# Performance work log

Hardware: AMD Instinct MI355X
Metric: run time of the kernel (lower is better)

## Reference

```python
import jax, jax.numpy as jnp
import numpy as np

B, S, D, H = 2, 2048, 1024, 4
DK = D // H


def setup_inputs() -> dict:
    key = jax.random.key(0)
    ks = jax.random.split(key, 12)
    inp = {
        "Q_input": jax.random.normal(ks[0], (B, S, D), jnp.float32),
        "K": jax.random.normal(ks[1], (B, S, D), jnp.float32),
        "V": jax.random.normal(ks[2], (B, S, D), jnp.float32),
        "T_field": jax.random.normal(ks[3], (32, 32, 16, 16), jnp.float32),
        "Wq_w": jax.random.normal(ks[4], (D, D), jnp.float32) * 0.02,
        "Wq_b": jnp.zeros((D,), jnp.float32),
        "Wo_w": jax.random.normal(ks[5], (D, D), jnp.float32) * 0.02,
        "Wo_b": jnp.zeros((D,), jnp.float32),
        "proj_w": jax.random.normal(ks[6], (24, DK), jnp.float32) * 0.02,
        "proj_b": jnp.zeros((24,), jnp.float32),
        "geo_w": jnp.ones((4,), jnp.float32),
        "temperature": jnp.asarray(1.0, jnp.float32),
    }
    return inp


def _psi(x, proj_w, proj_b):
    # x: (B,H,S,DK) -> 16D real biquaternion via (A,B,Theta) -> A*exp(Th)+B*exp(i*Th)
    gen = x @ proj_w.T + proj_b                      # (B,H,S,24)
    A, Bg = gen[..., 0:8], gen[..., 8:16]
    Th = jnp.clip(gen[..., 16:24], -8.0, 8.0)
    psi_real = A * jnp.exp(Th) + Bg * jnp.cos(Th)
    psi_imag = Bg * jnp.sin(Th)
    return jnp.concatenate([psi_real, psi_imag], axis=-1)  # (B,H,S,16)


def reference(Q_input, K, V, T_field, Wq_w, Wq_b, Wo_w, Wo_b, proj_w, proj_b, geo_w, temperature):
    b, sq, d = Q_input.shape
    sk = K.shape[1]
    dk = d // H
    Q = (Q_input @ Wq_w.T + Wq_b).reshape(b, sq, H, dk).transpose(0, 2, 1, 3)
    Kh = K.reshape(b, sk, H, dk).transpose(0, 2, 1, 3)
    Vh = V.reshape(b, sk, H, dk).transpose(0, 2, 1, 3)
    pq = _psi(Q, proj_w, proj_b)   # (b,H,sq,16)
    pk = _psi(Kh, proj_w, proj_b)  # (b,H,sk,16)
    qr, qi = pq[..., :8], pq[..., 8:]
    kr, ki = pk[..., :8], pk[..., 8:]
    # tensor: real part of complex inner product; spinor: imaginary (rotational) part
    tensor = jnp.einsum('bhqd,bhkd->bhqk', qr, kr) + jnp.einsum('bhqd,bhkd->bhqk', qi, ki)
    spinor = jnp.einsum('bhqd,bhkd->bhqk', qr, ki) - jnp.einsum('bhqd,bhkd->bhqk', qi, kr)
    qn2 = jnp.sum(pq * pq, -1)  # (b,H,sq)
    kn2 = jnp.sum(pk * pk, -1)  # (b,H,sk)
    gram = qn2[..., :, None] * kn2[..., None, :]
    # wedge: antisymmetric span magnitude (Gram residual)
    wedge = jnp.sqrt(jnp.maximum(gram - tensor**2 - spinor**2, 0.0) + 1e-6)
    # hodge: amplitude contraction (rank-2 -> rank-1 conservation)
    hodge = jnp.sqrt(qn2 + 1e-6)[..., :, None] * jnp.sqrt(kn2 + 1e-6)[..., None, :]
    scores = (geo_w[0] * wedge + geo_w[1] * tensor + geo_w[2] * spinor + geo_w[3] * hodge) / 4.0
    scores = scores / temperature
    w = jax.nn.softmax(scores, axis=-1)              # dropout disabled (eval)
    out = jnp.einsum('bhqk,bhkd->bhqd', w, Vh)
    out = out.transpose(0, 2, 1, 3).reshape(b, sq, d)
    return out @ Wo_w.T + Wo_b
```

## Files before the change

### kernel.cpp

```cpp
#include <hip/hip_runtime.h>
#include <hip/hip_bf16.h>
#include <math.h>

#define B_ 2
#define S_ 2048
#define D_ 1024
#define H_ 4
#define DK_ 256
#define NJ 24
#define NG 96
#define KTA 128
#define NT2 (S_ / KTA)
#define NTL (NT2 / 2)

typedef _Float16 f16;
typedef _Float16 f16x2 __attribute__((ext_vector_type(2)));
typedef _Float16 f16x4 __attribute__((ext_vector_type(4)));
typedef _Float16 f16x8 __attribute__((ext_vector_type(8)));
typedef float f32x16 __attribute__((ext_vector_type(16)));
typedef float v2f __attribute__((ext_vector_type(2)));

__global__ __launch_bounds__(256) void k_prep(
    const float* __restrict__ Wq_w, const float* __restrict__ proj_w,
    const float* __restrict__ Wq_b, const float* __restrict__ proj_b,
    const float* __restrict__ Wo_w, const float* __restrict__ V,
    f16* __restrict__ Mf, f16* __restrict__ Mkf,
    float* __restrict__ cbias, float* __restrict__ pbias,
    f16* __restrict__ Wf, f16* __restrict__ Vt2) {
  __shared__ f16 tile[64][72];
  const int bid = blockIdx.x;
  const int t = threadIdx.x;
  if (bid < 384) {
    int tid = bid * 256 + t;
    int hj = tid >> 10, d = tid & 1023;
    int h = hj / NJ, j = hj - h * NJ;
    const float* wq = Wq_w + (size_t)(h * DK_) * D_ + d;
    const float* pw = proj_w + j * DK_;
    float acc = 0.f;
#pragma unroll 8
    for (int k = 0; k < DK_; ++k) acc += wq[(size_t)k * D_] * pw[k];
    Mf[(size_t)hj * D_ + d] = (f16)acc;
  } else if (bid == 384) {
    if (t < NG) {
      int h = t / NJ, j = t - h * NJ;
      float acc = proj_b[j];
      for (int k = 0; k < DK_; ++k) acc += Wq_b[h * DK_ + k] * proj_w[j * DK_ + k];
      cbias[t] = acc;
      pbias[t] = proj_b[j];
    }
  } else if (bid < 769) {
    int tid = (bid - 385) * 256 + t;
    int hj = tid >> 10, d = tid & 1023;
    int h = hj / NJ, j = hj - h * NJ;
    float v = ((d >> 8) == h) ? proj_w[j * DK_ + (d & 255)] : 0.f;
    Mkf[tid] = (f16)v;
  } else if (bid < 1281) {
    int i = ((bid - 769) * 256 + t) * 8;
    float4 a = *(const float4*)(Wo_w + i);
    float4 b = *(const float4*)(Wo_w + i + 4);
    f16x8 o = {(f16)a.x, (f16)a.y, (f16)a.z, (f16)a.w,
               (f16)b.x, (f16)b.y, (f16)b.z, (f16)b.w};
    *(f16x8*)(Wf + i) = o;
  } else {
    int vbid = bid - 1281;
    int s0 = (vbid & 31) * 64, c0 = ((vbid >> 5) & 3) * 64;
    int bh = vbid >> 7;
    int b = bh >> 2, h = bh & 3;
    const float* src = V + (size_t)b * S_ * D_ + h * DK_ + c0;
#pragma unroll
    for (int u = 0; u < 4; ++u) {
      int row = (t >> 4) + 16 * u;
      int c4 = (t & 15) * 4;
      float4 v = *(const float4*)(src + (size_t)(s0 + row) * D_ + c4);
      tile[c4 + 0][row] = (f16)v.x;
      tile[c4 + 1][row] = (f16)v.y;
      tile[c4 + 2][row] = (f16)v.z;
      tile[c4 + 3][row] = (f16)v.w;
    }
    __syncthreads();
#pragma unroll
    for (int u = 0; u < 2; ++u) {
      int sid = t + 256 * u;
      int sgroup = sid & 7, dkl = sid >> 3;
      int dk = c0 + dkl, s = s0 + sgroup * 8;
      int wv = dk >> 5, qq = dk & 31;
      int kt = s >> 7, ks = (s >> 4) & 7, lhh = (s >> 3) & 1;
      size_t idx = ((((size_t)(bh * 8 + wv) * 16 + kt) * 8 + ks) * 2 + lhh) * 256 + qq * 8;
      *(f16x8*)(Vt2 + idx) = *(const f16x8*)&tile[dkl][sgroup * 8];
    }
  }
}

__global__ __launch_bounds__(256, 1) void k_gen(
    const float* __restrict__ Q, const float* __restrict__ Kin,
    const f16* __restrict__ Mf, const f16* __restrict__ Mkf,
    const float* __restrict__ cbias, const float* __restrict__ pbias,
    f16* __restrict__ pqF, float* __restrict__ qn2,
    f16* __restrict__ pkF, float* __restrict__ kn2) {
  __shared__ __align__(16) f16 Xs[8192];
  __shared__ __align__(16) f16 Bs[24576];
  __shared__ __align__(16) float redP[4][32][96];
  __shared__ float genL[32][100];

  const int t = threadIdx.x;
  const int w = t >> 6, lane = t & 63;
  const int l31 = lane & 31, lh = lane >> 5;
  const bool isQ = blockIdx.x < 128;
  const int r0 = (isQ ? blockIdx.x : blockIdx.x - 128) * 32;
  const float* X = isQ ? Q : Kin;
  const f16* Bf = isQ ? Mf : Mkf;
  const float* bias = isQ ? cbias : pbias;

  int xrow[8], xk4[8];
#pragma unroll
  for (int u = 0; u < 8; ++u) {
    int idx = t + 256 * u;
    xrow[u] = idx >> 6;
    xk4[u] = idx & 63;
  }
  int bcol[12], bkg[12];
#pragma unroll
  for (int u = 0; u < 12; ++u) {
    int idx = t + 256 * u;
    bcol[u] = idx >> 5;
    bkg[u] = idx & 31;
  }

  float4 xr[8];
  f16x8 br[12];
#define XLOAD(K0)                                                              \
  {                                                                            \
    _Pragma("unroll") for (int u = 0; u < 8; ++u) xr[u] =                      \
        *(const float4*)(X + (size_t)(r0 + xrow[u]) * D_ + (K0) + xk4[u] * 4); \
  }
#define BLOAD(K0)                                                            \
  {                                                                          \
    _Pragma("unroll") for (int u = 0; u < 12; ++u) br[u] =                   \
        *(const f16x8*)(Bf + (size_t)bcol[u] * D_ + (K0) + bkg[u] * 8);      \
  }
#define XWRITE()                                                            \
  {                                                                         \
    _Pragma("unroll") for (int u = 0; u < 8; ++u) {                         \
      f16x4 v = {(f16)xr[u].x, (f16)xr[u].y, (f16)xr[u].z, (f16)xr[u].w};   \
      *(f16x4*)&Xs[((xk4[u] >> 1) * 32 + xrow[u]) * 8 + (xk4[u] & 1) * 4] = v; \
    }                                                                       \
  }
#define BWRITE()                                                            \
  {                                                                         \
    _Pragma("unroll") for (int u = 0; u < 12; ++u)                          \
        *(f16x8*)&Bs[(bcol[u] >> 5) * 8192 + bkg[u] * 256 +                 \
                     (bcol[u] & 31) * 8] = br[u];                           \
  }

  XLOAD(0);
  BLOAD(0);
  XWRITE();
  BWRITE();
  __syncthreads();

  f32x16 acc0{}, acc1{}, acc2{};
  for (int ch = 0; ch < 4; ++ch) {
    if (ch < 3) {
      XLOAD((ch + 1) * 256);
      BLOAD((ch + 1) * 256);
    }
#pragma unroll
    for (int i = 0; i < 4; ++i) {
      const int kk = w * 4 + i;
      const int off = (kk * 2 + lh) * 256 + l31 * 8;
      f16x8 af = *(const f16x8*)&Xs[off];
      f16x8 b0 = *(const f16x8*)&Bs[off];
      f16x8 b1 = *(const f16x8*)&Bs[8192 + off];
      f16x8 b2 = *(const f16x8*)&Bs[16384 + off];
      acc0 = __builtin_amdgcn_mfma_f32_32x32x16_f16(af, b0, acc0, 0, 0, 0);
      acc1 = __builtin_amdgcn_mfma_f32_32x32x16_f16(af, b1, acc1, 0, 0, 0);
      acc2 = __builtin_amdgcn_mfma_f32_32x32x16_f16(af, b2, acc2, 0, 0, 0);
    }
    __syncthreads();
    if (ch < 3) {
      XWRITE();
      BWRITE();
      __syncthreads();
    }
  }
#undef XLOAD
#undef BLOAD
#undef XWRITE
#undef BWRITE

#pragma unroll
  for (int r = 0; r < 16; ++r) {
    const int row = (r & 3) + 8 * (r >> 2) + 4 * lh;
    redP[w][row][l31] = acc0[r];
    redP[w][row][32 + l31] = acc1[r];
    redP[w][row][64 + l31] = acc2[r];
  }
  __syncthreads();

  {
    const int row = t >> 3, cg = t & 7;
#pragma unroll
    for (int c = 0; c < 12; ++c) {
      int col = cg * 12 + c;
      genL[row][col] = redP[0][row][col] + redP[1][row][col] +
                       redP[2][row][col] + redP[3][row][col] + bias[col];
    }
  }
  __syncthreads();

  {
    const int rg = t >> 6;
    const int hh = (t & 63) >> 4;
    const int ii = t & 15;
    const int j = ii & 7;
    f16* po = isQ ? pqF : pkF;
    float* n2o = isQ ? qn2 : kn2;
#pragma unroll 2
    for (int r = 0; r < 8; ++r) {
      int row = rg * 8 + r;
      int g = r0 + row;
      int b = g >> 11, s = g & (S_ - 1);
      const float* gl = &genL[row][hh * NJ];
      float A = gl[j], Bg = gl[8 + j];
      float Th = fminf(fmaxf(gl[16 + j], -8.f), 8.f);
      float val = (ii < 8) ? (A * expf(Th) + Bg * cosf(Th)) : (Bg * sinf(Th));
      size_t base = (size_t)(b * H_ + hh) * S_ + s;
      po[base * 16 + ii] = (f16)val;
      float sq = val * val;
#pragma unroll
      for (int off = 1; off < 16; off <<= 1) sq += __shfl_xor(sq, off);
      if (ii == 0) n2o[base] = sq;
    }
  }
}

__global__ __launch_bounds__(256) void k_kmax(const float* __restrict__ kn2,
                                              float* __restrict__ khm) {
  __shared__ float red[4];
  const int bh = blockIdx.x, t = threadIdx.x;
  float m = 0.f;
#pragma unroll
  for (int u = 0; u < 8; ++u) m = fmaxf(m, kn2[(size_t)bh * S_ + t + 256 * u]);
#pragma unroll
  for (int off = 1; off < 64; off <<= 1) m = fmaxf(m, __shfl_xor(m, off));
  if ((t & 63) == 0) red[t >> 6] = m;
  __syncthreads();
  if (t == 0) {
    float mm = fmaxf(fmaxf(red[0], red[1]), fmaxf(red[2], red[3]));
    khm[bh] = sqrtf(mm + 1e-6f);
  }
}

__global__ __launch_bounds__(512, 4) void k_attn(
    const f16* __restrict__ pqF, const float* __restrict__ qn2,
    const f16* __restrict__ pkF, const float* __restrict__ kn2,
    const f16* __restrict__ Vt2, const float* __restrict__ geo_w,
    const float* __restrict__ temp, const float* __restrict__ khm,
    float* __restrict__ pacc, float* __restrict__ pml) {
  __shared__ __align__(16) float kn2s[2][KTA];
  __shared__ __align__(16) float khs[2][KTA];
  __shared__ float sPart[8][32];
  __shared__ __align__(16) f16 Plds[2][16][32][8];

  const int t = threadIdx.x;
  const int w = t >> 6;
  const int lane = t & 63;
  const int q_ = lane & 31;
  const int lh = lane >> 5;

  const int bid = blockIdx.x;
  const int half = bid >> 9;
  const int inner = bid & 511;
  const int bh = inner & 7, qt = inner >> 3;
  const int q0 = qt * 32;
  const int kofs = half * (S_ / 2);

  const size_t bhS = (size_t)bh * S_;
  const f16* pkb = pkF + bhS * 16;
  const float* kn2b = kn2 + bhS + kofs;

  const float scale = 0.25f / temp[0] * 1.4426950408889634f;
  const float g0s = geo_w[0] * scale, g1s = geo_w[1] * scale, g2s = geo_w[2] * scale;
  const float g3s = geo_w[3] * scale;

  const f16x8 bq = *(const f16x8*)(pqF + (bhS + q0 + q_) * 16 + lh * 8);
  const float qn2q = qn2[bhS + q0 + q_];
  const float qh = sqrtf(qn2q + 1e-6f);
  const float qh3 = qh * g3s;
  const float sumg = fabsf(g0s) + fabsf(g1s) + fabsf(g2s) + fabsf(g3s);
  const float Mhat = sumg * qh * khm[bh] - 4.328085123f;

  const v2f qn2v = {qn2q, qn2q};
  const v2f g0v = {g0s, g0s}, g1v = {g1s, g1s}, g2v = {g2s, g2s};
  const v2f zero2 = {0.f, 0.f}, eps2 = {1e-6f, 1e-6f};
  const v2f mhv = {Mhat, Mhat};

  const f16* ap_base = pkb + (size_t)(kofs + w * 16 + (q_ & 15)) * 16 +
                       ((q_ < 16) ? lh * 8 : (1 - lh) * 8);
  const f16* vb_lane = Vt2 + ((size_t)(bh * 8 + w) * 16 + half * NTL) * 4096 +
                       lh * 256 + q_ * 8;

  if (t < KTA) { float kv = kn2b[t]; kn2s[0][t] = kv; khs[0][t] = sqrtf(kv + 1e-6f); }
  float lreg = 0.f;
  f32x16 acc{};
  const f32x16 zacc{};

  f16x8 af = *(const f16x8*)ap_base;
  f16x8 bv[8];
#pragma unroll
  for (int ks = 0; ks < 8; ++ks) bv[ks] = *(const f16x8*)(vb_lane + ks * 512);
  __syncthreads();

  for (int ktl = 0; ktl < NTL; ++ktl) {
    const int k0l = ktl * KTA;
    const int cb = ktl & 1, nb = cb ^ 1;

    float knv = 0.f;
    if (t < KTA && ktl + 1 < NTL) knv = kn2b[k0l + KTA + t];

    f16x8 afx = af;
    if (q_ >= 16 && lh == 1) afx = -afx;
    __builtin_amdgcn_s_setprio(1);
    f32x16 sc = __builtin_amdgcn_mfma_f32_32x32x16_f16(afx, bq, zacc, 0, 0, 0);
    __builtin_amdgcn_s_setprio(0);
    if (ktl + 1 < NTL) af = *(const f16x8*)(ap_base + (size_t)(k0l + KTA) * 16);

    float pv[8];
    v2f psv = {0.f, 0.f};
#pragma unroll
    for (int rp = 0; rp < 4; ++rp) {
      const int r = 2 * rp;
      const int kb2 = w * 16 + 4 * lh + (rp & 1) * 2 + (rp >> 1) * 8;
      v2f tn = {sc[r], sc[r + 1]};
      v2f sp = {sc[r + 8], sc[r + 9]};
      v2f kn2p = *(const v2f*)&kn2s[cb][kb2];
      v2f khp = *(const v2f*)&khs[cb][kb2];
      v2f wr = qn2v * kn2p - tn * tn - sp * sp;
      wr = __builtin_elementwise_max(wr, zero2) + eps2;
      v2f wg = {sqrtf(wr.x), sqrtf(wr.y)};
      v2f sv2 = g0v * wg + g1v * tn + g2v * sp + qh3 * khp - mhv;
      v2f p2 = {exp2f(sv2.x), exp2f(sv2.y)};
      pv[r] = p2.x;
      pv[r + 1] = p2.y;
      psv += p2;
    }
    lreg += psv.x + psv.y;

    if (t < KTA && ktl + 1 < NTL) {
      kn2s[nb][t] = knv;
      khs[nb][t] = sqrtf(knv + 1e-6f);
    }
    {
      f16x2 p01 = {(f16)pv[0], (f16)pv[1]};
      f16x2 p23 = {(f16)pv[2], (f16)pv[3]};
      f16x2 p45 = {(f16)pv[4], (f16)pv[5]};
      f16x2 p67 = {(f16)pv[6], (f16)pv[7]};
      *(f16x2*)&Plds[cb][2 * w + 0][q_][4 * lh + 0] = p01;
      *(f16x2*)&Plds[cb][2 * w + 0][q_][4 * lh + 2] = p23;
      *(f16x2*)&Plds[cb][2 * w + 1][q_][4 * lh + 0] = p45;
      *(f16x2*)&Plds[cb][2 * w + 1][q_][4 * lh + 2] = p67;
    }
    __syncthreads();

    __builtin_amdgcn_s_setprio(1);
#pragma unroll
    for (int ks = 0; ks < 8; ++ks) {
      f16x8 pa = *(const f16x8*)&Plds[cb][2 * ks + lh][q_][0];
      acc = __builtin_amdgcn_mfma_f32_32x32x16_f16(pa, bv[ks], acc, 0, 0, 0);
    }
    __builtin_amdgcn_s_setprio(0);
    if (ktl + 1 < NTL) {
      const f16* vbn = vb_lane + (size_t)(ktl + 1) * 4096;
#pragma unroll
      for (int ks = 0; ks < 8; ++ks) bv[ks] = *(const f16x8*)(vbn + ks * 512);
    }
  }

  lreg += __shfl_xor(lreg, 32);
  if (lh == 0) sPart[w][q_] = lreg;
  __syncthreads();
  if (t < 32) {
    float s8 = 0.f;
#pragma unroll
    for (int i = 0; i < 8; ++i) s8 += sPart[i][t];
    pml[(size_t)bid * 64 + t] = s8;
  }
#pragma unroll
  for (int r = 0; r < 16; ++r) {
    const int row = (r & 3) + 8 * (r >> 2) + 4 * lh;
    pacc[((size_t)bid * 32 + row) * 256 + w * 32 + q_] = acc[r];
  }
}

__global__ __launch_bounds__(256) void k_merge(const float* __restrict__ pacc,
                                               const float* __restrict__ pml,
                                               f16* __restrict__ attnF) {
  const int inner = blockIdx.x;
  const int bh = inner & 7, qt = inner >> 3;
  const int b = bh >> 2, h = bh & 3;
  const int t = threadIdx.x;
  const int q = t >> 3, dgrp = t & 7;
  const float* a0 = pacc + ((size_t)inner * 32 + q) * 256 + dgrp * 32;
  const float* a1 = pacc + ((size_t)(inner + 512) * 32 + q) * 256 + dgrp * 32;
  const float l0 = pml[(size_t)inner * 64 + q];
  const float l1 = pml[(size_t)(inner + 512) * 64 + q];
  const float linv = 1.f / (l0 + l1);
  f16* dst = attnF + ((size_t)b * S_ + qt * 32 + q) * D_ + h * DK_ + dgrp * 32;
#pragma unroll
  for (int i = 0; i < 4; ++i) {
    float4 x0 = ((const float4*)a0)[2 * i];
    float4 y0 = ((const float4*)a0)[2 * i + 1];
    float4 x1 = ((const float4*)a1)[2 * i];
    float4 y1 = ((const float4*)a1)[2 * i + 1];
    f16x8 o = {(f16)((x0.x + x1.x) * linv), (f16)((x0.y + x1.y) * linv),
               (f16)((x0.z + x1.z) * linv), (f16)((x0.w + x1.w) * linv),
               (f16)((y0.x + y1.x) * linv), (f16)((y0.y + y1.y) * linv),
               (f16)((y0.z + y1.z) * linv), (f16)((y0.w + y1.w) * linv)};
    *(f16x8*)(dst + 8 * i) = o;
  }
}

__global__ __launch_bounds__(256, 1) void k_wo(const f16* __restrict__ A,
                                               const f16* __restrict__ Wt,
                                               const float* __restrict__ bias,
                                               float* __restrict__ C) {
  __shared__ __align__(16) f16 Abuf[2][128 * 64];
  __shared__ __align__(16) f16 Bbuf[2][128 * 64];
  const int t = threadIdx.x;
  const int w = t >> 6, lane = t & 63;
  const int wr = w >> 1, wc = w & 1;
  const int brow = blockIdx.y * 128, bcol = blockIdx.x * 128;

  int srow[4], skof[4];
#pragma unroll
  for (int u = 0; u < 4; ++u) {
    int c = t + 256 * u;
    int sub = c >> 6, l6 = c & 63;
    srow[u] = (sub >> 2) * 32 + (l6 & 31);
    skof[u] = (sub & 3) * 16 + (l6 >> 5) * 8;
  }

  uint4 ra0, ra1, ra2, ra3, rb0, rb1, rb2, rb3;
#define LOAD_TILE(K0)                                                        \
  {                                                                          \
    ra0 = *(const uint4*)(A + (size_t)(brow + srow[0]) * D_ + (K0) + skof[0]); \
    ra1 = *(const uint4*)(A + (size_t)(brow + srow[1]) * D_ + (K0) + skof[1]); \
    ra2 = *(const uint4*)(A + (size_t)(brow + srow[2]) * D_ + (K0) + skof[2]); \
    ra3 = *(const uint4*)(A + (size_t)(brow + srow[3]) * D_ + (K0) + skof[3]); \
    rb0 = *(const uint4*)(Wt + (size_t)(bcol + srow[0]) * D_ + (K0) + skof[0]); \
    rb1 = *(const uint4*)(Wt + (size_t)(bcol + srow[1]) * D_ + (K0) + skof[1]); \
    rb2 = *(const uint4*)(Wt + (size_t)(bcol + srow[2]) * D_ + (K0) + skof[2]); \
    rb3 = *(const uint4*)(Wt + (size_t)(bcol + srow[3]) * D_ + (K0) + skof[3]); \
  }
#define WRITE_TILE(BUF)                                       \
  {                                                           \
    *(uint4*)&Abuf[BUF][(t + 0) * 8] = ra0;                   \
    *(uint4*)&Abuf[BUF][(t + 256) * 8] = ra1;                 \
    *(uint4*)&Abuf[BUF][(t + 512) * 8] = ra2;                 \
    *(uint4*)&Abuf[BUF][(t + 768) * 8] = ra3;                 \
    *(uint4*)&Bbuf[BUF][(t + 0) * 8] = rb0;                   \
    *(uint4*)&Bbuf[BUF][(t + 256) * 8] = rb1;                 \
    *(uint4*)&Bbuf[BUF][(t + 512) * 8] = rb2;                 \
    *(uint4*)&Bbuf[BUF][(t + 768) * 8] = rb3;                 \
  }

  f32x16 acc00{}, acc01{}, acc10{}, acc11{};

  LOAD_TILE(0);
  WRITE_TILE(0);
  LOAD_TILE(64);
  __syncthreads();

  int cur = 0;
  for (int kt = 0; kt < 16; ++kt) {
    const int am0 = (wr * 2 + 0) * 4, am1 = (wr * 2 + 1) * 4;
    const int bn0 = (wc * 2 + 0) * 4, bn1 = (wc * 2 + 1) * 4;
#pragma unroll
    for (int kk = 0; kk < 4; ++kk) {
      f16x8 a0 = *(const f16x8*)&Abuf[cur][(am0 + kk) * 512 + lane * 8];
      f16x8 a1 = *(const f16x8*)&Abuf[cur][(am1 + kk) * 512 + lane * 8];
      f16x8 b0 = *(const f16x8*)&Bbuf[cur][(bn0 + kk) * 512 + lane * 8];
      f16x8 b1 = *(const f16x8*)&Bbuf[cur][(bn1 + kk) * 512 + lane * 8];
      acc00 = __builtin_amdgcn_mfma_f32_32x32x16_f16(a0, b0, acc00, 0, 0, 0);
      acc01 = __builtin_amdgcn_mfma_f32_32x32x16_f16(a0, b1, acc01, 0, 0, 0);
      acc10 = __builtin_amdgcn_mfma_f32_32x32x16_f16(a1, b0, acc10, 0, 0, 0);
      acc11 = __builtin_amdgcn_mfma_f32_32x32x16_f16(a1, b1, acc11, 0, 0, 0);
    }
    if (kt + 1 < 16) {
      WRITE_TILE(cur ^ 1);
      if (kt + 2 < 16) LOAD_TILE((kt + 2) * 64);
    }
    __syncthreads();
    cur ^= 1;
  }

  const int l31 = lane & 31, lh = lane >> 5;
  const float bv0 = bias[bcol + (wc * 2 + 0) * 32 + l31];
  const float bv1 = bias[bcol + (wc * 2 + 1) * 32 + l31];
#pragma unroll
  for (int r = 0; r < 16; ++r) {
    const int row = (r & 3) + 8 * (r >> 2) + 4 * lh;
    const size_t m0r = (size_t)(brow + (wr * 2 + 0) * 32 + row) * D_;
    const size_t m1r = (size_t)(brow + (wr * 2 + 1) * 32 + row) * D_;
    C[m0r + bcol + (wc * 2 + 0) * 32 + l31] = acc00[r] + bv0;
    C[m0r + bcol + (wc * 2 + 1) * 32 + l31] = acc01[r] + bv1;
    C[m1r + bcol + (wc * 2 + 0) * 32 + l31] = acc10[r] + bv0;
    C[m1r + bcol + (wc * 2 + 1) * 32 + l31] = acc11[r] + bv1;
  }
#undef LOAD_TILE
#undef WRITE_TILE
}

extern "C" void kernel_launch(void* const* d_in, const int* in_sizes, int n_in,
                              void* d_out, int out_size, void* d_ws, size_t ws_size,
                              hipStream_t stream) {
  const float* Q_input = (const float*)d_in[0];
  const float* K = (const float*)d_in[1];
  const float* V = (const float*)d_in[2];
  const float* Wq_w = (const float*)d_in[4];
  const float* Wq_b = (const float*)d_in[5];
  const float* Wo_w = (const float*)d_in[6];
  const float* Wo_b = (const float*)d_in[7];
  const float* proj_w = (const float*)d_in[8];
  const float* proj_b = (const float*)d_in[9];
  const float* geo_w = (const float*)d_in[10];
  const float* temp = (const float*)d_in[11];

  float* ws = (float*)d_ws;
  float* cbias = ws;
  float* pbias = cbias + 128;
  float* khm = pbias + 128;
  f16* Mf = (f16*)(khm + 128);
  f16* Mkf = Mf + 98304;
  float* qn2 = (float*)(Mkf + 98304);
  float* kn2 = qn2 + 16384;
  f16* pqF = (f16*)(kn2 + 16384);
  f16* pkF = pqF + 262144;
  f16* Vt2 = pkF + 262144;
  f16* attnF = Vt2 + 4194304;
  f16* Wf = attnF + 4194304;
  float* pacc = (float*)(Wf + 1048576);
  float* pml = pacc + 8388608;
  float* out = (float*)d_out;

  k_prep<<<dim3(2305), dim3(256), 0, stream>>>(Wq_w, proj_w, Wq_b, proj_b, Wo_w,
                                               V, Mf, Mkf, cbias, pbias, Wf, Vt2);
  k_gen<<<dim3(256), dim3(256), 0, stream>>>(Q_input, K, Mf, Mkf, cbias, pbias,
                                             pqF, qn2, pkF, kn2);
  k_kmax<<<dim3(8), dim3(256), 0, stream>>>(kn2, khm);
  k_attn<<<dim3(1024), dim3(512), 0, stream>>>(pqF, qn2, pkF, kn2, Vt2, geo_w,
                                               temp, khm, pacc, pml);
  k_merge<<<dim3(512), dim3(256), 0, stream>>>(pacc, pml, attnF);
  k_wo<<<dim3(8, 32), dim3(256), 0, stream>>>(attnF, Wf, Wo_b, out);
}
```

Baseline: 128.2 us.

## Drop split-K attention and merge kernel; fold key-norm max into generator

The attention kernel now walks the full key range in each block instead of splitting keys across two blocks. It normalizes and writes the f16 output directly, which removes the fp32 partial-accumulator round trip and the separate merge kernel. The per-head max of key norms is now computed with atomicMax inside the generator kernel, with khm zeroed in the prep kernel, and the separate reduction kernel is gone. The trade-off is half as many attention blocks (512 vs 1024), so there is less parallelism and a longer serial loop per block, in exchange for fewer launches and less memory traffic.

```diff
diff --git a/kernel.cpp b/kernel.cpp
--- a/kernel.cpp
+++ b/kernel.cpp
@@ -11,7 +11,6 @@
 #define NG 96
 #define KTA 128
 #define NT2 (S_ / KTA)
-#define NTL (NT2 / 2)
 
 typedef _Float16 f16;
 typedef _Float16 f16x2 __attribute__((ext_vector_type(2)));
@@ -26,7 +25,7 @@
     const float* __restrict__ Wo_w, const float* __restrict__ V,
     f16* __restrict__ Mf, f16* __restrict__ Mkf,
     float* __restrict__ cbias, float* __restrict__ pbias,
-    f16* __restrict__ Wf, f16* __restrict__ Vt2) {
+    f16* __restrict__ Wf, f16* __restrict__ Vt2, float* __restrict__ khm) {
   __shared__ f16 tile[64][72];
   const int bid = blockIdx.x;
   const int t = threadIdx.x;
@@ -48,6 +47,7 @@
       cbias[t] = acc;
       pbias[t] = proj_b[j];
     }
+    if (t < 8) ((unsigned int*)khm)[t] = 0u;
   } else if (bid < 769) {
     int tid = (bid - 385) * 256 + t;
     int hj = tid >> 10, d = tid & 1023;
@@ -96,7 +96,8 @@
     const f16* __restrict__ Mf, const f16* __restrict__ Mkf,
     const float* __restrict__ cbias, const float* __restrict__ pbias,
     f16* __restrict__ pqF, float* __restrict__ qn2,
-    f16* __restrict__ pkF, float* __restrict__ kn2) {
+    f16* __restrict__ pkF, float* __restrict__ kn2,
+    float* __restrict__ khm) {
   __shared__ __align__(16) f16 Xs[8192];
   __shared__ __align__(16) f16 Bs[24576];
   __shared__ __align__(16) float redP[4][32][96];
@@ -215,6 +216,7 @@
     const int j = ii & 7;
     f16* po = isQ ? pqF : pkF;
     float* n2o = isQ ? qn2 : kn2;
+    float mx = 0.f;
 #pragma unroll 2
     for (int r = 0; r < 8; ++r) {
       int row = rg * 8 + r;
@@ -229,25 +231,16 @@
       float sq = val * val;
 #pragma unroll
       for (int off = 1; off < 16; off <<= 1) sq += __shfl_xor(sq, off);
-      if (ii == 0) n2o[base] = sq;
-    }
-  }
-}
-
-__global__ __launch_bounds__(256) void k_kmax(const float* __restrict__ kn2,
-                                              float* __restrict__ khm) {
-  __shared__ float red[4];
-  const int bh = blockIdx.x, t = threadIdx.x;
-  float m = 0.f;
-#pragma unroll
-  for (int u = 0; u < 8; ++u) m = fmaxf(m, kn2[(size_t)bh * S_ + t + 256 * u]);
-#pragma unroll
-  for (int off = 1; off < 64; off <<= 1) m = fmaxf(m, __shfl_xor(m, off));
-  if ((t & 63) == 0) red[t >> 6] = m;
-  __syncthreads();
-  if (t == 0) {
-    float mm = fmaxf(fmaxf(red[0], red[1]), fmaxf(red[2], red[3]));
-    khm[bh] = sqrtf(mm + 1e-6f);
+      if (ii == 0) {
+        n2o[base] = sq;
+        mx = fmaxf(mx, sq);
+      }
+    }
+    if (!isQ && ii == 0) {
+      int g = r0;
+      int b = g >> 11;
+      atomicMax((unsigned int*)&khm[b * H_ + hh], __float_as_uint(mx));
+    }
   }
 }
 
@@ -256,10 +249,11 @@
     const f16* __restrict__ pkF, const float* __restrict__ kn2,
     const f16* __restrict__ Vt2, const float* __restrict__ geo_w,
     const float* __restrict__ temp, const float* __restrict__ khm,
-    float* __restrict__ pacc, float* __restrict__ pml) {
+    f16* __restrict__ attnF) {
   __shared__ __align__(16) float kn2s[2][KTA];
   __shared__ __align__(16) float khs[2][KTA];
   __shared__ float sPart[8][32];
+  __shared__ float linvL[32];
   __shared__ __align__(16) f16 Plds[2][16][32][8];
 
   const int t = threadIdx.x;
@@ -269,15 +263,13 @@
   const int lh = lane >> 5;
 
   const int bid = blockIdx.x;
-  const int half = bid >> 9;
-  const int inner = bid & 511;
-  const int bh = inner & 7, qt = inner >> 3;
+  const int bh = bid & 7, qt = bid >> 3;
   const int q0 = qt * 32;
-  const int kofs = half * (S_ / 2);
+  const int b = bh >> 2, h = bh & 3;
 
   const size_t bhS = (size_t)bh * S_;
   const f16* pkb = pkF + bhS * 16;
-  const float* kn2b = kn2 + bhS + kofs;
+  const float* kn2b = kn2 + bhS;
 
   const float scale = 0.25f / temp[0] * 1.4426950408889634f;
   const float g0s = geo_w[0] * scale, g1s = geo_w[1] * scale, g2s = geo_w[2] * scale;
@@ -288,17 +280,16 @@
   const float qh = sqrtf(qn2q + 1e-6f);
   const float qh3 = qh * g3s;
   const float sumg = fabsf(g0s) + fabsf(g1s) + fabsf(g2s) + fabsf(g3s);
-  const float Mhat = sumg * qh * khm[bh] - 4.328085123f;
+  const float Mhat = sumg * qh * sqrtf(khm[bh] + 1e-6f) - 4.328085123f;
 
   const v2f qn2v = {qn2q, qn2q};
   const v2f g0v = {g0s, g0s}, g1v = {g1s, g1s}, g2v = {g2s, g2s};
   const v2f zero2 = {0.f, 0.f}, eps2 = {1e-6f, 1e-6f};
   const v2f mhv = {Mhat, Mhat};
 
-  const f16* ap_base = pkb + (size_t)(kofs + w * 16 + (q_ & 15)) * 16 +
+  const f16* ap_base = pkb + (size_t)(w * 16 + (q_ & 15)) * 16 +
                        ((q_ < 16) ? lh * 8 : (1 - lh) * 8);
-  const f16* vb_lane = Vt2 + ((size_t)(bh * 8 + w) * 16 + half * NTL) * 4096 +
-                       lh * 256 + q_ * 8;
+  const f16* vb_lane = Vt2 + (size_t)(bh * 8 + w) * 16 * 4096 + lh * 256 + q_ * 8;
 
   if (t < KTA) { float kv = kn2b[t]; kn2s[0][t] = kv; khs[0][t] = sqrtf(kv + 1e-6f); }
   float lreg = 0.f;
@@ -311,19 +302,19 @@
   for (int ks = 0; ks < 8; ++ks) bv[ks] = *(const f16x8*)(vb_lane + ks * 512);
   __syncthreads();
 
-  for (int ktl = 0; ktl < NTL; ++ktl) {
+  for (int ktl = 0; ktl < NT2; ++ktl) {
     const int k0l = ktl * KTA;
     const int cb = ktl & 1, nb = cb ^ 1;
 
     float knv = 0.f;
-    if (t < KTA && ktl + 1 < NTL) knv = kn2b[k0l + KTA + t];
+    if (t < KTA && ktl + 1 < NT2) knv = kn2b[k0l + KTA + t];
 
     f16x8 afx = af;
     if (q_ >= 16 && lh == 1) afx = -afx;
     __builtin_amdgcn_s_setprio(1);
     f32x16 sc = __builtin_amdgcn_mfma_f32_32x32x16_f16(afx, bq, zacc, 0, 0, 0);
     __builtin_amdgcn_s_setprio(0);
-    if (ktl + 1 < NTL) af = *(const f16x8*)(ap_base + (size_t)(k0l + KTA) * 16);
+    if (ktl + 1 < NT2) af = *(const f16x8*)(ap_base + (size_t)(k0l + KTA) * 16);
 
     float pv[8];
     v2f psv = {0.f, 0.f};
@@ -346,7 +337,7 @@
     }
     lreg += psv.x + psv.y;
 
-    if (t < KTA && ktl + 1 < NTL) {
+    if (t < KTA && ktl + 1 < NT2) {
       kn2s[nb][t] = knv;
       khs[nb][t] = sqrtf(knv + 1e-6f);
     }
@@ -369,7 +360,7 @@
       acc = __builtin_amdgcn_mfma_f32_32x32x16_f16(pa, bv[ks], acc, 0, 0, 0);
     }
     __builtin_amdgcn_s_setprio(0);
-    if (ktl + 1 < NTL) {
+    if (ktl + 1 < NT2) {
       const f16* vbn = vb_lane + (size_t)(ktl + 1) * 4096;
 #pragma unroll
       for (int ks = 0; ks < 8; ++ks) bv[ks] = *(const f16x8*)(vbn + ks * 512);
@@ -383,40 +374,14 @@
     float s8 = 0.f;
 #pragma unroll
     for (int i = 0; i < 8; ++i) s8 += sPart[i][t];
-    pml[(size_t)bid * 64 + t] = s8;
-  }
+    linvL[t] = 1.f / s8;
+  }
+  __syncthreads();
+  const size_t obase = ((size_t)b * S_ + q0) * D_ + h * DK_ + w * 32 + q_;
 #pragma unroll
   for (int r = 0; r < 16; ++r) {
     const int row = (r & 3) + 8 * (r >> 2) + 4 * lh;
-    pacc[((size_t)bid * 32 + row) * 256 + w * 32 + q_] = acc[r];
-  }
-}
-
-__global__ __launch_bounds__(256) void k_merge(const float* __restrict__ pacc,
-                                               const float* __restrict__ pml,
-                                               f16* __restrict__ attnF) {
-  const int inner = blockIdx.x;
-  const int bh = inner & 7, qt = inner >> 3;
-  const int b = bh >> 2, h = bh & 3;
-  const int t = threadIdx.x;
-  const int q = t >> 3, dgrp = t & 7;
-  const float* a0 = pacc + ((size_t)inner * 32 + q) * 256 + dgrp * 32;
-  const float* a1 = pacc + ((size_t)(inner + 512) * 32 + q) * 256 + dgrp * 32;
-  const float l0 = pml[(size_t)inner * 64 + q];
-  const float l1 = pml[(size_t)(inner + 512) * 64 + q];
-  const float linv = 1.f / (l0 + l1);
-  f16* dst = attnF + ((size_t)b * S_ + qt * 32 + q) * D_ + h * DK_ + dgrp * 32;
-#pragma unroll
-  for (int i = 0; i < 4; ++i) {
-    float4 x0 = ((const float4*)a0)[2 * i];
-    float4 y0 = ((const float4*)a0)[2 * i + 1];
-    float4 x1 = ((const float4*)a1)[2 * i];
-    float4 y1 = ((const float4*)a1)[2 * i + 1];
-    f16x8 o = {(f16)((x0.x + x1.x) * linv), (f16)((x0.y + x1.y) * linv),
-               (f16)((x0.z + x1.z) * linv), (f16)((x0.w + x1.w) * linv),
-               (f16)((y0.x + y1.x) * linv), (f16)((y0.y + y1.y) * linv),
-               (f16)((y0.z + y1.z) * linv), (f16)((y0.w + y1.w) * linv)};
-    *(f16x8*)(dst + 8 * i) = o;
+    attnF[obase + (size_t)row * D_] = (f16)(acc[r] * linvL[row]);
   }
 }
 
@@ -539,17 +504,14 @@
   f16* Vt2 = pkF + 262144;
   f16* attnF = Vt2 + 4194304;
   f16* Wf = attnF + 4194304;
-  float* pacc = (float*)(Wf + 1048576);
-  float* pml = pacc + 8388608;
   float* out = (float*)d_out;
 
   k_prep<<<dim3(2305), dim3(256), 0, stream>>>(Wq_w, proj_w, Wq_b, proj_b, Wo_w,
-                                               V, Mf, Mkf, cbias, pbias, Wf, Vt2);
+                                               V, Mf, Mkf, cbias, pbias, Wf, Vt2,
+                                               khm);
   k_gen<<<dim3(256), dim3(256), 0, stream>>>(Q_input, K, Mf, Mkf, cbias, pbias,
-                                             pqF, qn2, pkF, kn2);
-  k_kmax<<<dim3(8), dim3(256), 0, stream>>>(kn2, khm);
-  k_attn<<<dim3(1024), dim3(512), 0, stream>>>(pqF, qn2, pkF, kn2, Vt2, geo_w,
-                                               temp, khm, pacc, pml);
-  k_merge<<<dim3(512), dim3(256), 0, stream>>>(pacc, pml, attnF);
+                                             pqF, qn2, pkF, kn2, khm);
+  k_attn<<<dim3(512), dim3(512), 0, stream>>>(pqF, qn2, pkF, kn2, Vt2, geo_w,
+                                              temp, khm, attnF);
   k_wo<<<dim3(8, 32), dim3(256), 0, stream>>>(attnF, Wf, Wo_b, out);
 }
```

Result: faster. 115.9 us (-9.6%).
